# Kernel tuning notes

Hardware: AMD Instinct MI355X
Metric: run time of the kernel (lower is better)

The kernel has to match this reference:

```python
import jax, jax.numpy as jnp
import numpy as np

B, T, D = 4, 4096, 1024

def setup_inputs() -> dict:
    key = jax.random.key(0)
    kx, kq, kk, kv = jax.random.split(key, 4)
    return {
        "x": jax.random.normal(kx, (B, T, D), dtype=jnp.float32),
        "w_q": jax.random.normal(kq, (D, D), dtype=jnp.float32),
        "w_k": jax.random.normal(kk, (D, D), dtype=jnp.float32),
        "w_v": jax.random.normal(kv, (D, D), dtype=jnp.float32),
    }

def reference(x, w_q, w_k, w_v):
    # Projections: (B,T,D) @ (D,D) -> (B,T,D)
    q = jnp.einsum('btk,kd->btd', x, w_q)
    k = jnp.einsum('btk,kd->btd', x, w_k)
    v = jnp.einsum('btk,kd->btd', x, w_v)
    d = x.shape[-1]
    # Faithful to source: gamma = 1/sqrt(1/d) = sqrt(d) (multiplies, not divides)
    gamma = jnp.sqrt(jnp.asarray(d, dtype=x.dtype))
    a = jnp.einsum('bqd,bkd->bqk', q, k) * gamma  # (B,T,T), no softmax
    y = jnp.einsum('bqt,btd->bqd', a, v)          # (B,T,D)
    return y
```

## Files before the change

### kernel.cpp

```cpp
#include <hip/hip_runtime.h>
#include <hip/hip_bf16.h>


typedef __attribute__((ext_vector_type(8))) short bf16x8;
typedef __attribute__((ext_vector_type(4))) float f32x4;

__device__ __forceinline__ unsigned short bf16bits(float f) {
    union { __hip_bfloat16 b; unsigned short s; } r;
    r.b = __float2bfloat16(f);
    return r.s;
}

__device__ __forceinline__ void gload16(const void* g, void* l) {
    __builtin_amdgcn_global_load_lds((__attribute__((address_space(1))) void*)g,
                                     (__attribute__((address_space(3))) void*)l,
                                     16, 0, 0);
}

template<int MODE, bool OUT_F32>
__global__ __launch_bounds__(512, 2)
void gemm8(const __hip_bfloat16* __restrict__ Ap, const __hip_bfloat16* __restrict__ Bp,
           void* __restrict__ Cp, int N, int Kc, int ldA, int ldB,
           long sA, long sB, long sC, int nb, int tnc, float scale)
{
    constexpr int BM = 256, BN = 128, BK = 64;
    __shared__ __hip_bfloat16 lds[3][(BM + BN) * BK];

    const int h = blockIdx.x;
    int slice, tile;
    if (MODE == 1) { slice = h & 7; tile = h >> 3; }
    else {
        const int xcd = h & 7;
        slice = xcd % nb;
        tile  = (xcd / nb) * ((int)gridDim.x >> 3) + (h >> 3);
    }
    const int batch = slice % nb, kc = slice / nb;
    const int n0 = (tile % tnc) * BN;
    const int m0 = (tile / tnc) * BM;

    const int tid  = threadIdx.x;
    const int lane = tid & 63;
    const int w    = tid >> 6;
    const int wm = (w >> 1) * 64, wn = (w & 1) * 64;
    const int l16 = lane & 15, lq = lane >> 4;

    const int srow = lane >> 3;
    const int scol = ((lane & 7) ^ srow) << 3;
    const int soff = w * 512 + lane * 8;

    const __hip_bfloat16* Ab = Ap + (size_t)batch * sA + (size_t)kc * Kc;
    const __hip_bfloat16* Bb = Bp + (size_t)batch * sB + (size_t)kc * Kc;

    const int nt = Kc >> 6;
    auto stage = [&](int buf, int t) {
        const int k0 = (t < nt ? t : nt - 1) << 6;
        __hip_bfloat16* L = &lds[buf][0];
        #pragma unroll
        for (int i = 0; i < 4; ++i)
            gload16(Ab + (size_t)(m0 + i * 64 + w * 8 + srow) * ldA + k0 + scol,
                    L + i * 4096 + soff);
        #pragma unroll
        for (int i = 0; i < 2; ++i)
            gload16(Bb + (size_t)(n0 + i * 64 + w * 8 + srow) * ldB + k0 + scol,
                    L + BM * BK + i * 4096 + soff);
    };

    f32x4 acc[4][4];
    #pragma unroll
    for (int i = 0; i < 4; ++i)
        #pragma unroll
        for (int j = 0; j < 4; ++j)
            acc[i][j] = (f32x4){0.f, 0.f, 0.f, 0.f};

    stage(0, 0);
    stage(1, 1);

    for (int t = 0; t < nt; ++t) {
        asm volatile("s_waitcnt vmcnt(6)" ::: "memory");
        __builtin_amdgcn_s_barrier();
        asm volatile("" ::: "memory");
        stage((t + 2) % 3, t + 2);

        const __hip_bfloat16* LA = &lds[t % 3][0];
        const __hip_bfloat16* LB = LA + BM * BK;
        #pragma unroll
        for (int kk = 0; kk < 2; ++kk) {
            const int sc = ((kk * 4 + lq) ^ (l16 & 7)) << 3;
            bf16x8 av[4], bv[4];
            #pragma unroll
            for (int i = 0; i < 4; ++i)
                av[i] = *(const bf16x8*)&LA[(wm + i * 16 + l16) * BK + sc];
            #pragma unroll
            for (int j = 0; j < 4; ++j)
                bv[j] = *(const bf16x8*)&LB[(wn + j * 16 + l16) * BK + sc];
            __builtin_amdgcn_s_setprio(1);
            #pragma unroll
            for (int i = 0; i < 4; ++i)
                #pragma unroll
                for (int j = 0; j < 4; ++j)
                    acc[i][j] = __builtin_amdgcn_mfma_f32_16x16x32_bf16(av[i], bv[j], acc[i][j], 0, 0, 0);
            __builtin_amdgcn_s_setprio(0);
        }
    }
    asm volatile("s_waitcnt vmcnt(0)" ::: "memory");

    float* Cf = (float*)Cp;
    __hip_bfloat16* Ch = (__hip_bfloat16*)Cp;
    const size_t cb0 = (size_t)slice * sC;
    #pragma unroll
    for (int i = 0; i < 4; ++i) {
        #pragma unroll
        for (int j = 0; j < 4; ++j) {
            const int row0 = m0 + wm + i * 16 + lq * 4;
            const int col  = n0 + wn + j * 16 + l16;
            #pragma unroll
            for (int r = 0; r < 4; ++r) {
                float v = acc[i][j][r] * scale;
                size_t idx = cb0 + (size_t)(row0 + r) * N + col;
                if (OUT_F32) Cf[idx] = v;
                else         Ch[idx] = __float2bfloat16(v);
            }
        }
    }
}

template<int TM, int TN, int MODE, bool OUT_F32>
__global__ __launch_bounds__(256)
void gemm_nt(const __hip_bfloat16* __restrict__ Ap, const __hip_bfloat16* __restrict__ Bp,
             void* __restrict__ Cp, int N, int Kc, int ldA, int ldB,
             long sA, long sB, long sC, int nb, float scale)
{
    constexpr int FM = TM / 32;
    constexpr int FN = TN / 32;

    __shared__ __hip_bfloat16 At[2][TM][32];
    __shared__ __hip_bfloat16 Bt[2][TN][32];

    const int gx = (int)gridDim.x, gy = (int)gridDim.y, gz = (int)gridDim.z;
    int slice, tile;
    if (MODE == 0) {
        slice = blockIdx.z;
        int wg = blockIdx.y * gx + blockIdx.x;
        const int cpx = (gx * gy) >> 3;
        tile = (wg & 7) * cpx + (wg >> 3);
    } else {
        const int h = ((int)blockIdx.z * gy + (int)blockIdx.y) * gx + (int)blockIdx.x;
        const int xcd = h & 7, k = h >> 3;
        if (MODE == 1) {
            const int SL = gz >> 3;
            slice = xcd + 8 * (k % SL);
            tile  = k / SL;
        } else {
            slice = xcd % gz;
            tile  = (xcd / gz) * ((gx * gy * gz) >> 3) + k;
        }
    }
    const int batch = slice % nb;
    const int kc    = slice / nb;
    const int n0 = (tile % gx) * TN;
    const int m0 = (tile / gx) * TM;

    const int tid  = threadIdx.x;
    const int lane = tid & 63;
    const int wave = tid >> 6;
    const int wm = (wave & 1) * (TM / 2);
    const int wn = (wave >> 1) * (TN / 2);
    const int l16 = lane & 15;
    const int lq  = lane >> 4;

    const int aoff = wave * (TM * 8) + lane * 8;
    const int boff = wave * (TN * 8) + lane * 8;
    const int arow = aoff >> 5, brow = boff >> 5;
    const int acs = (((aoff >> 3) & 3) ^ ((aoff >> 6) & 3)) << 3;
    const int bcs = (((boff >> 3) & 3) ^ ((boff >> 6) & 3)) << 3;
    const int sc = (lq ^ ((l16 >> 1) & 3)) << 3;

    const __hip_bfloat16* Ab = Ap + (size_t)batch * sA + (size_t)kc * Kc;
    const __hip_bfloat16* Bb = Bp + (size_t)batch * sB + (size_t)kc * Kc;

    auto stage = [&](int buf, int k0) {
        #pragma unroll
        for (int i = 0; i < TM / 64; ++i)
            gload16(Ab + (size_t)(m0 + arow + i * 16) * ldA + k0 + acs,
                    &At[buf][0][0] + aoff + i * 512);
        #pragma unroll
        for (int i = 0; i < TN / 64; ++i)
            gload16(Bb + (size_t)(n0 + brow + i * 16) * ldB + k0 + bcs,
                    &Bt[buf][0][0] + boff + i * 512);
    };

    f32x4 acc[FM][FN];
    #pragma unroll
    for (int i = 0; i < FM; ++i)
        #pragma unroll
        for (int j = 0; j < FN; ++j)
            acc[i][j] = (f32x4){0.f, 0.f, 0.f, 0.f};

    stage(0, 0);
    __syncthreads();

    const int nt = Kc >> 5;
    for (int t = 0; t < nt; ++t) {
        const int cur = t & 1;
        if (t + 1 < nt) stage(cur ^ 1, (t + 1) << 5);

        bf16x8 av[FM], bv[FN];
        #pragma unroll
        for (int i = 0; i < FM; ++i)
            av[i] = *(const bf16x8*)&At[cur][wm + i * 16 + l16][sc];
        #pragma unroll
        for (int j = 0; j < FN; ++j)
            bv[j] = *(const bf16x8*)&Bt[cur][wn + j * 16 + l16][sc];
        #pragma unroll
        for (int i = 0; i < FM; ++i)
            #pragma unroll
            for (int j = 0; j < FN; ++j)
                acc[i][j] = __builtin_amdgcn_mfma_f32_16x16x32_bf16(av[i], bv[j], acc[i][j], 0, 0, 0);
        __syncthreads();
    }

    float* Cf = (float*)Cp;
    __hip_bfloat16* Ch = (__hip_bfloat16*)Cp;
    const size_t cb0 = (size_t)slice * sC;
    #pragma unroll
    for (int i = 0; i < FM; ++i) {
        #pragma unroll
        for (int j = 0; j < FN; ++j) {
            const int row0 = m0 + wm + i * 16 + lq * 4;
            const int col  = n0 + wn + j * 16 + l16;
            #pragma unroll
            for (int r = 0; r < 4; ++r) {
                float v = acc[i][j][r] * scale;
                size_t idx = cb0 + (size_t)(row0 + r) * N + col;
                if (OUT_F32) Cf[idx] = v;
                else         Ch[idx] = __float2bfloat16(v);
            }
        }
    }
}

__global__ __launch_bounds__(256)
void reduce_kchunks(const unsigned short* __restrict__ part,
                    unsigned short* __restrict__ out)
{
    const size_t l = ((size_t)blockIdx.x * 256 + threadIdx.x) * 8;
    const size_t DD4 = (size_t)4 << 20;
    union { unsigned short h[8]; uint4 u; } a, b, o;
    a.u = *(const uint4*)(part + l);
    b.u = *(const uint4*)(part + l + DD4);
    #pragma unroll
    for (int j = 0; j < 8; ++j) {
        union { float f; unsigned int u; } fa, fb;
        fa.u = (unsigned int)a.h[j] << 16;
        fb.u = (unsigned int)b.h[j] << 16;
        o.h[j] = bf16bits(fa.f + fb.f);
    }
    *(uint4*)(out + l) = o.u;
}

#define TP 64
__global__ __launch_bounds__(256)
void transpose_cast(const float* __restrict__ in, __hip_bfloat16* __restrict__ out,
                    __hip_bfloat16* __restrict__ straight, int nsb,
                    int R, int C, long inStride, long outStride)
{
    __shared__ __hip_bfloat16 t2[TP][TP + 4];
    const int b  = blockIdx.z;
    const int r0 = blockIdx.x * TP;
    const int c0 = blockIdx.y * TP;
    const float* inb = in + (size_t)b * inStride;
    __hip_bfloat16* outb = out + (size_t)b * outStride;
    __hip_bfloat16* stb  = straight + (size_t)b * inStride;
    const int t  = threadIdx.x;
    const int rr = t >> 4;
    const int c4 = (t & 15) * 4;
    #pragma unroll
    for (int p = 0; p < 4; ++p) {
        const int row = p * 16 + rr;
        float4 f = *(const float4*)&inb[(size_t)(r0 + row) * C + c0 + c4];
        union { __hip_bfloat16 h[4]; uint2 u; } s;
        s.h[0] = __float2bfloat16(f.x); s.h[1] = __float2bfloat16(f.y);
        s.h[2] = __float2bfloat16(f.z); s.h[3] = __float2bfloat16(f.w);
        t2[c4 + 0][row] = s.h[0];
        t2[c4 + 1][row] = s.h[1];
        t2[c4 + 2][row] = s.h[2];
        t2[c4 + 3][row] = s.h[3];
        if (b < nsb)
            *(uint2*)&stb[(size_t)(r0 + row) * C + c0 + c4] = s.u;
    }
    __syncthreads();
    #pragma unroll
    for (int p = 0; p < 4; ++p) {
        const int crow = p * 16 + rr;
        union { __hip_bfloat16 h[4]; uint2 u; } o;
        #pragma unroll
        for (int j = 0; j < 4; ++j) o.h[j] = t2[crow][c4 + j];
        *(uint2*)&outb[(size_t)(c0 + crow) * R + r0 + c4] = o.u;
    }
}

__global__ __launch_bounds__(256)
void cast_f32_bf16(const float* __restrict__ in, __hip_bfloat16* __restrict__ out, int n)
{
    const int i = (blockIdx.x * 256 + threadIdx.x) << 2;
    if (i >= n) return;
    float4 f = *(const float4*)(in + i);
    union { __hip_bfloat16 h[4]; uint2 u; } t;
    t.h[0] = __float2bfloat16(f.x); t.h[1] = __float2bfloat16(f.y);
    t.h[2] = __float2bfloat16(f.z); t.h[3] = __float2bfloat16(f.w);
    *(uint2*)(out + i) = t.u;
}

extern "C" void kernel_launch(void* const* d_in, const int* in_sizes, int n_in,
                              void* d_out, int out_size, void* d_ws, size_t ws_size,
                              hipStream_t stream)
{
    const int Bz = 4, T = 4096, D = 1024;
    const float gamma = 32.0f;

    const float* x  = (const float*)d_in[0];
    const float* wq = (const float*)d_in[1];
    const float* wk = (const float*)d_in[2];
    const float* wv = (const float*)d_in[3];
    float* y = (float*)d_out;

    unsigned char* p = (unsigned char*)d_ws;
    const size_t DD = (size_t)D * D;
    __hip_bfloat16* Gb  = (__hip_bfloat16*)p; p += Bz * DD * 2;
    __hip_bfloat16* Hb  = (__hip_bfloat16*)p; p += Bz * DD * 2;
    __hip_bfloat16* PTb = (__hip_bfloat16*)p; p += Bz * DD * 2;
    __hip_bfloat16* wqb = (__hip_bfloat16*)p; p += DD * 2;
    __hip_bfloat16* wkb = (__hip_bfloat16*)p; p += DD * 2;
    __hip_bfloat16* wvT = (__hip_bfloat16*)p; p += DD * 2;
    __hip_bfloat16* C0b = (__hip_bfloat16*)p; p += DD * 2;
    __hip_bfloat16* Gpart = Hb;
    __hip_bfloat16* xb23  = Gb;

    __hip_bfloat16* xbT  = (__hip_bfloat16*)d_out;
    __hip_bfloat16* xb01 = (__hip_bfloat16*)((unsigned char*)d_out + ((size_t)32 << 20));

    dim3 blk(256);

    cast_f32_bf16<<<dim3((int)(DD / 1024)), blk, 0, stream>>>(wq, wqb, (int)DD);
    cast_f32_bf16<<<dim3((int)(DD / 1024)), blk, 0, stream>>>(wk, wkb, (int)DD);
    transpose_cast<<<dim3(D / TP, D / TP, 1), blk, 0, stream>>>(
        wv, wvT, wvT, 0, D, D, 0, 0);
    transpose_cast<<<dim3(T / TP, D / TP, Bz), blk, 0, stream>>>(
        x, xbT, xb01, 2, T, D, (long)T * D, (long)D * T);

    gemm_nt<64, 128, 0, false><<<dim3(D / 128, D / 64, 1), blk, 0, stream>>>(
        wqb, wkb, C0b, D, D, D, D, 0, 0, 0, 1, 1.0f);
    gemm8<1, false><<<dim3(256), dim3(512), 0, stream>>>(
        xbT, xbT, Gpart, D, T / 2, T, T, (long)D * T, (long)D * T, (long)DD, Bz, 8, 1.0f);
    reduce_kchunks<<<dim3((int)(Bz * DD / 2048)), blk, 0, stream>>>(
        (const unsigned short*)Gpart, (unsigned short*)Gb);
    gemm_nt<64, 128, 2, false><<<dim3(D / 128, D / 64, Bz), blk, 0, stream>>>(
        C0b, Gb, Hb, D, D, D, D, 0, (long)DD, (long)DD, Bz, 1.0f);
    gemm_nt<64, 128, 2, false><<<dim3(D / 128, D / 64, Bz), blk, 0, stream>>>(
        wvT, Hb, PTb, D, D, D, D, 0, (long)DD, (long)DD, Bz, gamma);

    cast_f32_bf16<<<dim3((int)(2 * (size_t)T * D / 1024)), blk, 0, stream>>>(
        x + (size_t)2 * T * D, xb23, (int)(2 * (size_t)T * D));

    gemm8<2, true><<<dim3(256), dim3(512), 0, stream>>>(
        xb01, PTb, y, D, D, D, D, (long)T * D, (long)DD, (long)T * D, 2, 8, 1.0f);
    gemm8<2, true><<<dim3(256), dim3(512), 0, stream>>>(
        xb23, PTb + 2 * DD, y + (size_t)2 * T * D, D, D, D, D,
        (long)T * D, (long)DD, (long)T * D, 2, 8, 1.0f);
}
```

Before: 275.6 us.

## Interleave gemm8 staging with MFMA halves and fuse casts into transpose pass

The gemm8 main loop now issues its global-to-LDS prefetch in two halves, one per kk sub-step. Barriers and explicit lgkmcnt waits are placed around each MFMA block so loads overlap compute more finely. Separately, the wq/wk casts are merged into one launch, and the x[2:4] bf16 cast is folded into the transpose kernel by writing the straight copy for all batches. Workspace buffers are remapped into d_out and shared scratch to fit the extra data. The extra barriers per sub-step add sync cost, and the aliasing of buffers like Hb in d_out risks overlap hazards.

```diff
diff --git a/kernel.cpp b/kernel.cpp
--- a/kernel.cpp
+++ b/kernel.cpp
@@ -52,17 +52,18 @@
     const __hip_bfloat16* Bb = Bp + (size_t)batch * sB + (size_t)kc * Kc;
 
     const int nt = Kc >> 6;
-    auto stage = [&](int buf, int t) {
+    auto stageH = [&](int t, int half) {
         const int k0 = (t < nt ? t : nt - 1) << 6;
-        __hip_bfloat16* L = &lds[buf][0];
-        #pragma unroll
-        for (int i = 0; i < 4; ++i)
-            gload16(Ab + (size_t)(m0 + i * 64 + w * 8 + srow) * ldA + k0 + scol,
-                    L + i * 4096 + soff);
-        #pragma unroll
-        for (int i = 0; i < 2; ++i)
-            gload16(Bb + (size_t)(n0 + i * 64 + w * 8 + srow) * ldB + k0 + scol,
-                    L + BM * BK + i * 4096 + soff);
+        __hip_bfloat16* L = &lds[t % 3][0];
+        if (half == 0) {
+            gload16(Ab + (size_t)(m0 +   0 + w * 8 + srow) * ldA + k0 + scol, L + 0 * 4096 + soff);
+            gload16(Ab + (size_t)(m0 +  64 + w * 8 + srow) * ldA + k0 + scol, L + 1 * 4096 + soff);
+            gload16(Bb + (size_t)(n0 +   0 + w * 8 + srow) * ldB + k0 + scol, L + BM * BK + 0 * 4096 + soff);
+        } else {
+            gload16(Ab + (size_t)(m0 + 128 + w * 8 + srow) * ldA + k0 + scol, L + 2 * 4096 + soff);
+            gload16(Ab + (size_t)(m0 + 192 + w * 8 + srow) * ldA + k0 + scol, L + 3 * 4096 + soff);
+            gload16(Bb + (size_t)(n0 +  64 + w * 8 + srow) * ldB + k0 + scol, L + BM * BK + 1 * 4096 + soff);
+        }
     };
 
     f32x4 acc[4][4];
@@ -72,15 +73,13 @@
         for (int j = 0; j < 4; ++j)
             acc[i][j] = (f32x4){0.f, 0.f, 0.f, 0.f};
 
-    stage(0, 0);
-    stage(1, 1);
+    stageH(0, 0); stageH(0, 1);
+    stageH(1, 0); stageH(1, 1);
+    asm volatile("s_waitcnt vmcnt(6)" ::: "memory");
+    __builtin_amdgcn_s_barrier();
+    asm volatile("" ::: "memory");
 
     for (int t = 0; t < nt; ++t) {
-        asm volatile("s_waitcnt vmcnt(6)" ::: "memory");
-        __builtin_amdgcn_s_barrier();
-        asm volatile("" ::: "memory");
-        stage((t + 2) % 3, t + 2);
-
         const __hip_bfloat16* LA = &lds[t % 3][0];
         const __hip_bfloat16* LB = LA + BM * BK;
         #pragma unroll
@@ -93,6 +92,12 @@
             #pragma unroll
             for (int j = 0; j < 4; ++j)
                 bv[j] = *(const bf16x8*)&LB[(wn + j * 16 + l16) * BK + sc];
+            stageH(t + 2, kk);
+            if (kk == 1)
+                asm volatile("s_waitcnt vmcnt(6)" ::: "memory");
+            __builtin_amdgcn_s_barrier();
+            asm volatile("s_waitcnt lgkmcnt(0)" ::: "memory");
+            __builtin_amdgcn_sched_barrier(0);
             __builtin_amdgcn_s_setprio(1);
             #pragma unroll
             for (int i = 0; i < 4; ++i)
@@ -100,6 +105,8 @@
                 for (int j = 0; j < 4; ++j)
                     acc[i][j] = __builtin_amdgcn_mfma_f32_16x16x32_bf16(av[i], bv[j], acc[i][j], 0, 0, 0);
             __builtin_amdgcn_s_setprio(0);
+            __builtin_amdgcn_s_barrier();
+            asm volatile("" ::: "memory");
         }
     }
     asm volatile("s_waitcnt vmcnt(0)" ::: "memory");
@@ -261,8 +268,8 @@
 #define TP 64
 __global__ __launch_bounds__(256)
 void transpose_cast(const float* __restrict__ in, __hip_bfloat16* __restrict__ out,
-                    __hip_bfloat16* __restrict__ straight, int nsb,
-                    int R, int C, long inStride, long outStride)
+                    __hip_bfloat16* __restrict__ s01, __hip_bfloat16* __restrict__ s23,
+                    int nsb, int R, int C, long inStride, long outStride)
 {
     __shared__ __hip_bfloat16 t2[TP][TP + 4];
     const int b  = blockIdx.z;
@@ -270,7 +277,8 @@
     const int c0 = blockIdx.y * TP;
     const float* inb = in + (size_t)b * inStride;
     __hip_bfloat16* outb = out + (size_t)b * outStride;
-    __hip_bfloat16* stb  = straight + (size_t)b * inStride;
+    __hip_bfloat16* stb  = (b < 2) ? s01 + (size_t)b * inStride
+                                   : s23 + (size_t)(b - 2) * inStride;
     const int t  = threadIdx.x;
     const int rr = t >> 4;
     const int c4 = (t & 15) * 4;
@@ -300,15 +308,18 @@
 }
 
 __global__ __launch_bounds__(256)
-void cast_f32_bf16(const float* __restrict__ in, __hip_bfloat16* __restrict__ out, int n)
-{
+void cast_qk(const float* __restrict__ wq, const float* __restrict__ wk,
+             __hip_bfloat16* __restrict__ out, int n)
+{
+    const float* src = blockIdx.y ? wk : wq;
+    __hip_bfloat16* dst = out + (size_t)blockIdx.y * n;
     const int i = (blockIdx.x * 256 + threadIdx.x) << 2;
     if (i >= n) return;
-    float4 f = *(const float4*)(in + i);
+    float4 f = *(const float4*)(src + i);
     union { __hip_bfloat16 h[4]; uint2 u; } t;
     t.h[0] = __float2bfloat16(f.x); t.h[1] = __float2bfloat16(f.y);
     t.h[2] = __float2bfloat16(f.z); t.h[3] = __float2bfloat16(f.w);
-    *(uint2*)(out + i) = t.u;
+    *(uint2*)(dst + i) = t.u;
 }
 
 extern "C" void kernel_launch(void* const* d_in, const int* in_sizes, int n_in,
@@ -326,27 +337,28 @@
 
     unsigned char* p = (unsigned char*)d_ws;
     const size_t DD = (size_t)D * D;
-    __hip_bfloat16* Gb  = (__hip_bfloat16*)p; p += Bz * DD * 2;
-    __hip_bfloat16* Hb  = (__hip_bfloat16*)p; p += Bz * DD * 2;
-    __hip_bfloat16* PTb = (__hip_bfloat16*)p; p += Bz * DD * 2;
-    __hip_bfloat16* wqb = (__hip_bfloat16*)p; p += DD * 2;
-    __hip_bfloat16* wkb = (__hip_bfloat16*)p; p += DD * 2;
-    __hip_bfloat16* wvT = (__hip_bfloat16*)p; p += DD * 2;
-    __hip_bfloat16* C0b = (__hip_bfloat16*)p; p += DD * 2;
-    __hip_bfloat16* Gpart = Hb;
-    __hip_bfloat16* xb23  = Gb;
-
-    __hip_bfloat16* xbT  = (__hip_bfloat16*)d_out;
-    __hip_bfloat16* xb01 = (__hip_bfloat16*)((unsigned char*)d_out + ((size_t)32 << 20));
+    __hip_bfloat16* S0  = (__hip_bfloat16*)p;
+    __hip_bfloat16* S2  = (__hip_bfloat16*)(p + ((size_t)16 << 20));
+    __hip_bfloat16* wqb = (__hip_bfloat16*)(p + ((size_t)24 << 20));
+    __hip_bfloat16* wkb = wqb + DD;
+    __hip_bfloat16* wvT = wkb + DD;
+    __hip_bfloat16* C0b = wvT + DD;
+    __hip_bfloat16* xb23 = S0;
+
+    __hip_bfloat16* xbT   = (__hip_bfloat16*)d_out;
+    __hip_bfloat16* xb01  = (__hip_bfloat16*)((unsigned char*)d_out + ((size_t)32 << 20));
+    __hip_bfloat16* Gpart = (__hip_bfloat16*)((unsigned char*)d_out + ((size_t)48 << 20));
+    __hip_bfloat16* Hb    = (__hip_bfloat16*)d_out;
+    __hip_bfloat16* Gb    = S2;
+    __hip_bfloat16* PTb   = S2;
 
     dim3 blk(256);
 
-    cast_f32_bf16<<<dim3((int)(DD / 1024)), blk, 0, stream>>>(wq, wqb, (int)DD);
-    cast_f32_bf16<<<dim3((int)(DD / 1024)), blk, 0, stream>>>(wk, wkb, (int)DD);
+    cast_qk<<<dim3((int)(DD / 1024), 2), blk, 0, stream>>>(wq, wk, wqb, (int)DD);
     transpose_cast<<<dim3(D / TP, D / TP, 1), blk, 0, stream>>>(
-        wv, wvT, wvT, 0, D, D, 0, 0);
+        wv, wvT, wvT, wvT, 0, D, D, 0, 0);
     transpose_cast<<<dim3(T / TP, D / TP, Bz), blk, 0, stream>>>(
-        x, xbT, xb01, 2, T, D, (long)T * D, (long)D * T);
+        x, xbT, xb01, xb23, 4, T, D, (long)T * D, (long)D * T);
 
     gemm_nt<64, 128, 0, false><<<dim3(D / 128, D / 64, 1), blk, 0, stream>>>(
         wqb, wkb, C0b, D, D, D, D, 0, 0, 0, 1, 1.0f);
@@ -359,9 +371,6 @@
     gemm_nt<64, 128, 2, false><<<dim3(D / 128, D / 64, Bz), blk, 0, stream>>>(
         wvT, Hb, PTb, D, D, D, D, 0, (long)DD, (long)DD, Bz, gamma);
 
-    cast_f32_bf16<<<dim3((int)(2 * (size_t)T * D / 1024)), blk, 0, stream>>>(
-        x + (size_t)2 * T * D, xb23, (int)(2 * (size_t)T * D));
-
     gemm8<2, true><<<dim3(256), dim3(512), 0, stream>>>(
         xb01, PTb, y, D, D, D, D, (long)T * D, (long)DD, (long)T * D, 2, 8, 1.0f);
     gemm8<2, true><<<dim3(256), dim3(512), 0, stream>>>(
```

Result: no change. 271.4 us (-1.5%).
